# Performance work log

Hardware: AMD Instinct MI355X
Metric: run time of the kernel (lower is better)

Reference implementation:

```python
import math
import jax, jax.numpy as jnp
import numpy as np

HEADS = 16


def setup_inputs() -> dict:
    key = jax.random.key(0)
    k1, k2, k3 = jax.random.split(key, 3)
    bs, n_ctx, width = 2, 2048, 1024
    x = jax.random.normal(k1, (bs, n_ctx, width), dtype=jnp.float32)
    # init_scale=0.25 style small init for stability
    W_qkv = jax.random.normal(k2, (width, 3 * width), dtype=jnp.float32) * (0.25 / math.sqrt(width))
    b_qkv = jnp.zeros((3 * width,), dtype=jnp.float32)
    W_proj = jax.random.normal(k3, (width, width), dtype=jnp.float32) * (0.25 / math.sqrt(width))
    b_proj = jnp.zeros((width,), dtype=jnp.float32)
    return {"x": x, "W_qkv": W_qkv, "b_qkv": b_qkv, "W_proj": W_proj, "b_proj": b_proj}


def reference(x, W_qkv, b_qkv, W_proj, b_proj):
    bs, n_ctx, width = x.shape
    qkv = x @ W_qkv + b_qkv                     # [b, s, 3*width]
    attn_ch = width // HEADS                    # head dim
    qkv = qkv.reshape(bs, n_ctx, HEADS, 3 * attn_ch)
    q, k, v = jnp.split(qkv, 3, axis=-1)        # each [b, s, h, c]
    scale = 1.0 / math.sqrt(math.sqrt(attn_ch)) # applied to both q and k
    weight = jnp.einsum('bthc,bshc->bhts', q * scale, k * scale)
    weight = jax.nn.softmax(weight.astype(jnp.float32), axis=-1).astype(qkv.dtype)
    out = jnp.einsum('bhts,bshc->bthc', weight, v).reshape(bs, n_ctx, width)
    return out @ W_proj + b_proj
```

## Files before the change

### kernel.cpp

```cpp
#include <hip/hip_runtime.h>


using u16 = unsigned short;
typedef __attribute__((ext_vector_type(8))) short s16x8;
typedef __attribute__((ext_vector_type(4))) float f32x4;
typedef __attribute__((ext_vector_type(16))) float f32x16;

__device__ __forceinline__ u16 f2bf(float f) {
    unsigned x = __builtin_bit_cast(unsigned, f);
    x += 0x7fffu + ((x >> 16) & 1u);
    return (u16)(x >> 16);
}
__device__ __forceinline__ float bf2f(u16 u) {
    return __builtin_bit_cast(float, ((unsigned)u) << 16);
}

#define MFMA(a, b, c)   __builtin_amdgcn_mfma_f32_16x16x32_bf16((a), (b), (c), 0, 0, 0)
#define MFMA32(a, b, c) __builtin_amdgcn_mfma_f32_32x32x16_bf16((a), (b), (c), 0, 0, 0)


__global__ __launch_bounds__(256) void convert_split(const float* __restrict__ in,
                                                     u16* __restrict__ H, u16* __restrict__ L, int n) {
    int i = (blockIdx.x * 256 + threadIdx.x) * 4;
    if (i >= n) return;
    float4 v = *(const float4*)(in + i);
    u16 h0 = f2bf(v.x), h1 = f2bf(v.y), h2 = f2bf(v.z), h3 = f2bf(v.w);
    ushort4 hh = { h0, h1, h2, h3 };
    ushort4 ll = { f2bf(v.x - bf2f(h0)), f2bf(v.y - bf2f(h1)), f2bf(v.z - bf2f(h2)), f2bf(v.w - bf2f(h3)) };
    *(ushort4*)(H + i) = hh;
    *(ushort4*)(L + i) = ll;
}

__global__ __launch_bounds__(256) void transpose_split(const float* __restrict__ W,
                                                       u16* __restrict__ TH, u16* __restrict__ TL,
                                                       int K, int N) {
    __shared__ float st[32][33];
    int n0 = blockIdx.x * 32, k0 = blockIdx.y * 32;
    int c = threadIdx.x & 31, r8 = threadIdx.x >> 5;
#pragma unroll
    for (int i = 0; i < 4; ++i) {
        int r = r8 + i * 8;
        st[r][c] = W[(size_t)(k0 + r) * N + n0 + c];
    }
    __syncthreads();
#pragma unroll
    for (int i = 0; i < 4; ++i) {
        int r = r8 + i * 8;
        float v = st[c][r];
        u16 h = f2bf(v);
        TH[(size_t)(n0 + r) * K + k0 + c] = h;
        TL[(size_t)(n0 + r) * K + k0 + c] = f2bf(v - bf2f(h));
    }
}


template <int EPI>
__global__ __launch_bounds__(256, 2) void gemm_bf16x3(
    const u16* __restrict__ AH, const u16* __restrict__ AL,
    const u16* __restrict__ BTH, const u16* __restrict__ BTL,
    const float* __restrict__ bias,
    u16* __restrict__ Qs, u16* __restrict__ Kb, u16* __restrict__ Vp,
    float* __restrict__ Out) {
    const int K = 1024;
    __shared__ u16 sAh[128][40], sAl[128][40], sBh[128][40], sBl[128][40];

    int m0 = blockIdx.y * 128, n0 = blockIdx.x * 128;
    int tid = threadIdx.x, lane = tid & 63, wv = tid >> 6;
    int g = lane >> 4, c16 = lane & 15;
    int wm = wv >> 1, wn = wv & 1;

    f32x4 acc[4][4] = {};

    for (int kt = 0; kt < 32; ++kt) {
        int k0 = kt * 32;
        s16x8 ra[2], rla[2], rb[2], rlb[2];
#pragma unroll
        for (int i = 0; i < 2; ++i) {
            int cc = i * 256 + tid;
            int rr = cc >> 2, ko = (cc & 3) * 8;
            ra[i]  = *(const s16x8*)(AH  + (size_t)(m0 + rr) * K + k0 + ko);
            rla[i] = *(const s16x8*)(AL  + (size_t)(m0 + rr) * K + k0 + ko);
            rb[i]  = *(const s16x8*)(BTH + (size_t)(n0 + rr) * K + k0 + ko);
            rlb[i] = *(const s16x8*)(BTL + (size_t)(n0 + rr) * K + k0 + ko);
        }
        __syncthreads();
#pragma unroll
        for (int i = 0; i < 2; ++i) {
            int cc = i * 256 + tid;
            int rr = cc >> 2, ko = (cc & 3) * 8;
            *(s16x8*)&sAh[rr][ko] = ra[i];
            *(s16x8*)&sAl[rr][ko] = rla[i];
            *(s16x8*)&sBh[rr][ko] = rb[i];
            *(s16x8*)&sBl[rr][ko] = rlb[i];
        }
        __syncthreads();

        s16x8 ah[4], al[4], bh[4], bl[4];
#pragma unroll
        for (int mi = 0; mi < 4; ++mi) {
            ah[mi] = *(const s16x8*)&sAh[wm * 64 + mi * 16 + c16][g * 8];
            al[mi] = *(const s16x8*)&sAl[wm * 64 + mi * 16 + c16][g * 8];
        }
#pragma unroll
        for (int ni = 0; ni < 4; ++ni) {
            bh[ni] = *(const s16x8*)&sBh[wn * 64 + ni * 16 + c16][g * 8];
            bl[ni] = *(const s16x8*)&sBl[wn * 64 + ni * 16 + c16][g * 8];
        }
#pragma unroll
        for (int mi = 0; mi < 4; ++mi)
#pragma unroll
            for (int ni = 0; ni < 4; ++ni) {
                f32x4 c = acc[mi][ni];
                c = MFMA(ah[mi], bh[ni], c);
                c = MFMA(al[mi], bh[ni], c);
                c = MFMA(ah[mi], bl[ni], c);
                acc[mi][ni] = c;
            }
    }

#pragma unroll
    for (int ni = 0; ni < 4; ++ni) {
        int col = n0 + wn * 64 + ni * 16 + c16;
        float bs = bias[col];
        if (EPI == 0) {
            int h = col / 192;
            int rm = col - h * 192;
#pragma unroll
            for (int mi = 0; mi < 4; ++mi)
#pragma unroll
                for (int r = 0; r < 4; ++r) {
                    int row = m0 + wm * 64 + mi * 16 + 4 * g + r;
                    int b = row >> 11, s = row & 2047;
                    int bh16 = b * 16 + h;
                    float val = acc[mi][ni][r] + bs;
                    if (rm < 64)
                        Qs[(((size_t)bh16 * 2048 + s) << 6) + rm] = f2bf(val * 0.125f);
                    else if (rm < 128)
                        Kb[(((size_t)bh16 * 2048 + s) << 6) + rm - 64] = f2bf(val);
                    else {
                        int d = rm - 128;
                        int kg = s >> 4, k16 = s & 15;
                        int mm = (k16 & 3) | (((k16 >> 3) & 1) << 2) | (((k16 >> 2) & 1) << 3);
                        Vp[(((size_t)bh16 * 128 + kg) * 64 + d) * 16 + mm] = f2bf(val);
                    }
                }
        } else {
#pragma unroll
            for (int mi = 0; mi < 4; ++mi)
#pragma unroll
                for (int r = 0; r < 4; ++r) {
                    int row = m0 + wm * 64 + mi * 16 + 4 * g + r;
                    Out[(size_t)row * 1024 + col] = acc[mi][ni][r] + bs;
                }
        }
    }
}

__global__ __launch_bounds__(256, 2) void attn_fwd(
    const u16* __restrict__ Qs, const u16* __restrict__ Kb, const u16* __restrict__ Vp,
    u16* __restrict__ OH, u16* __restrict__ OL) {
    int id = blockIdx.x;
    int xcd = id & 7, li = id >> 3;
    int bh = xcd * 4 + (li >> 4);
    int qb = li & 15;
    int tid = threadIdx.x, w = tid >> 6, lane = tid & 63;
    int l31 = lane & 31, h = lane >> 5;
    int q0 = (qb * 4 + w) * 32;

    size_t base = (size_t)bh * 2048 * 64;
    size_t vbase = (size_t)bh * 128 * 64 * 16;

    const u16* qp = Qs + base + (size_t)(q0 + l31) * 64 + 8 * h;
    s16x8 qf0 = *(const s16x8*)(qp);
    s16x8 qf1 = *(const s16x8*)(qp + 16);
    s16x8 qf2 = *(const s16x8*)(qp + 32);
    s16x8 qf3 = *(const s16x8*)(qp + 48);

    const u16* kp = Kb + base + (size_t)l31 * 64 + 8 * h;
    const u16* vb = Vp + vbase + (size_t)l31 * 16 + 8 * h;

    f32x16 o0 = {}, o1 = {};
    float m = -1e30f, ls = 0.f;

    s16x8 ka0, ka1, ka2, ka3, kb0, kb1, kb2, kb3;
    ka0 = *(const s16x8*)(kp);
    ka1 = *(const s16x8*)(kp + 16);
    ka2 = *(const s16x8*)(kp + 32);
    ka3 = *(const s16x8*)(kp + 48);

    auto step = [&](s16x8& c0, s16x8& c1, s16x8& c2, s16x8& c3,
                    s16x8& n0, s16x8& n1, s16x8& n2, s16x8& n3,
                    int kv, int kvn) {
        const u16* vp = vb + (size_t)(kv >> 4) * 1024;
        s16x8 v00 = *(const s16x8*)(vp);
        s16x8 v10 = *(const s16x8*)(vp + 512);
        s16x8 v01 = *(const s16x8*)(vp + 1024);
        s16x8 v11 = *(const s16x8*)(vp + 1536);

        f32x16 s = {};
        s = MFMA32(c0, qf0, s);
        s = MFMA32(c1, qf1, s);
        s = MFMA32(c2, qf2, s);
        s = MFMA32(c3, qf3, s);

        const u16* kpn = kp + (size_t)kvn * 64;
        n0 = *(const s16x8*)(kpn);
        n1 = *(const s16x8*)(kpn + 16);
        n2 = *(const s16x8*)(kpn + 32);
        n3 = *(const s16x8*)(kpn + 48);

        float pmax = s[0];
#pragma unroll
        for (int r = 1; r < 16; ++r) pmax = fmaxf(pmax, s[r]);
        pmax = fmaxf(pmax, __shfl_xor(pmax, 32));

        if (!__all(pmax <= m + 8.f)) {
            float mn = fmaxf(m, pmax);
            float f = __expf(m - mn);
            m = mn;
            ls *= f;
#pragma unroll
            for (int r = 0; r < 16; ++r) {
                float fb = __shfl(f, (r & 3) + 8 * (r >> 2) + 4 * h);
                o0[r] *= fb;
                o1[r] *= fb;
            }
        }

        float sm = 0.f;
        u16 pb[16];
#pragma unroll
        for (int r = 0; r < 16; ++r) {
            float e = __expf(s[r] - m);
            sm += e;
            pb[r] = f2bf(e);
        }
        sm += __shfl_xor(sm, 32);
        ls += sm;

        s16x8 pa0, pa1;
#pragma unroll
        for (int e = 0; e < 8; ++e) {
            pa0[e] = (short)pb[e];
            pa1[e] = (short)pb[8 + e];
        }

        o0 = MFMA32(pa0, v00, o0);
        o0 = MFMA32(pa1, v01, o0);
        o1 = MFMA32(pa0, v10, o1);
        o1 = MFMA32(pa1, v11, o1);
    };

    for (int j = 0; j < 64; j += 2) {
        step(ka0, ka1, ka2, ka3, kb0, kb1, kb2, kb3, j * 32, (j + 1) * 32);
        step(kb0, kb1, kb2, kb3, ka0, ka1, ka2, ka3, (j + 1) * 32, ((j + 2) & 63) * 32);
    }

    int b = bh >> 4, hh = bh & 15;
    float inv = 1.0f / ls;
#pragma unroll
    for (int r = 0; r < 16; ++r) {
        int cr = (r & 3) + 8 * (r >> 2) + 4 * h;
        float fb = __shfl(inv, cr);
        int row = q0 + cr;
        size_t idx = ((size_t)(b * 2048 + row)) * 1024 + hh * 64 + l31;
        float v0 = o0[r] * fb, v1 = o1[r] * fb;
        u16 h0 = f2bf(v0);
        OH[idx] = h0;
        OL[idx] = f2bf(v0 - bf2f(h0));
        u16 h1 = f2bf(v1);
        OH[idx + 32] = h1;
        OL[idx + 32] = f2bf(v1 - bf2f(h1));
    }
}


extern "C" void kernel_launch(void* const* d_in, const int* in_sizes, int n_in,
                              void* d_out, int out_size, void* d_ws, size_t ws_size,
                              hipStream_t stream) {
    const float* x     = (const float*)d_in[0];
    const float* Wqkv  = (const float*)d_in[1];
    const float* bqkv  = (const float*)d_in[2];
    const float* Wproj = (const float*)d_in[3];
    const float* bproj = (const float*)d_in[4];
    float* out = (float*)d_out;

    char* w = (char*)d_ws;
    const size_t SZ_X  = (size_t)4096 * 1024 * 2;
    const size_t SZ_WQ = (size_t)3072 * 1024 * 2;
    const size_t SZ_WP = (size_t)1024 * 1024 * 2;
    u16* XH  = (u16*)w; w += SZ_X;
    u16* XL  = (u16*)w; w += SZ_X;
    u16* WQH = (u16*)w; w += SZ_WQ;
    u16* WQL = (u16*)w; w += SZ_WQ;
    u16* WPH = (u16*)w; w += SZ_WP;
    u16* WPL = (u16*)w; w += SZ_WP;
    u16* Q_s = (u16*)w; w += SZ_X;
    u16* K_b = (u16*)w; w += SZ_X;
    u16* V_p = (u16*)w; w += SZ_X;
    u16* OHp = (u16*)w; w += SZ_X;
    u16* OLp = (u16*)w; w += SZ_X;

    convert_split<<<4096, 256, 0, stream>>>(x, XH, XL, 4096 * 1024);
    transpose_split<<<dim3(96, 32), 256, 0, stream>>>(Wqkv, WQH, WQL, 1024, 3072);
    transpose_split<<<dim3(32, 32), 256, 0, stream>>>(Wproj, WPH, WPL, 1024, 1024);
    gemm_bf16x3<0><<<dim3(24, 32), 256, 0, stream>>>(XH, XL, WQH, WQL, bqkv, Q_s, K_b, V_p, nullptr);
    attn_fwd<<<512, 256, 0, stream>>>(Q_s, K_b, V_p, OHp, OLp);
    gemm_bf16x3<1><<<dim3(8, 32), 256, 0, stream>>>(OHp, OLp, WPH, WPL, bproj, nullptr, nullptr, nullptr, out);
}
```

Measured before the change: 214.2 us.

## Process 64 keys per attention step, fold log2e into Q, use exp2

```diff
diff --git a/kernel.cpp b/kernel.cpp
--- a/kernel.cpp
+++ b/kernel.cpp
@@ -13,6 +13,13 @@
 }
 __device__ __forceinline__ float bf2f(u16 u) {
     return __builtin_bit_cast(float, ((unsigned)u) << 16);
+}
+__device__ __forceinline__ unsigned pk2bf(float lo, float hi) {
+    unsigned a = __builtin_bit_cast(unsigned, lo);
+    unsigned b = __builtin_bit_cast(unsigned, hi);
+    a += 0x7fffu + ((a >> 16) & 1u);
+    b += 0x7fffu + ((b >> 16) & 1u);
+    return (a >> 16) | (b & 0xffff0000u);
 }
 
 #define MFMA(a, b, c)   __builtin_amdgcn_mfma_f32_16x16x32_bf16((a), (b), (c), 0, 0, 0)
@@ -134,7 +141,7 @@
                     int bh16 = b * 16 + h;
                     float val = acc[mi][ni][r] + bs;
                     if (rm < 64)
-                        Qs[(((size_t)bh16 * 2048 + s) << 6) + rm] = f2bf(val * 0.125f);
+                        Qs[(((size_t)bh16 * 2048 + s) << 6) + rm] = f2bf(val * 0.18033688011112042f);
                     else if (rm < 128)
                         Kb[(((size_t)bh16 * 2048 + s) << 6) + rm - 64] = f2bf(val);
                     else {
@@ -168,13 +175,12 @@
     int q0 = (qb * 4 + w) * 32;
 
     size_t base = (size_t)bh * 2048 * 64;
-    size_t vbase = (size_t)bh * 128 * 64 * 16;
+    size_t vbase = (size_t)bh * 131072;
 
     const u16* qp = Qs + base + (size_t)(q0 + l31) * 64 + 8 * h;
-    s16x8 qf0 = *(const s16x8*)(qp);
-    s16x8 qf1 = *(const s16x8*)(qp + 16);
-    s16x8 qf2 = *(const s16x8*)(qp + 32);
-    s16x8 qf3 = *(const s16x8*)(qp + 48);
+    s16x8 qf[4];
+#pragma unroll
+    for (int c = 0; c < 4; ++c) qf[c] = *(const s16x8*)(qp + 16 * c);
 
     const u16* kp = Kb + base + (size_t)l31 * 64 + 8 * h;
     const u16* vb = Vp + vbase + (size_t)l31 * 16 + 8 * h;
@@ -182,41 +188,53 @@
     f32x16 o0 = {}, o1 = {};
     float m = -1e30f, ls = 0.f;
 
-    s16x8 ka0, ka1, ka2, ka3, kb0, kb1, kb2, kb3;
-    ka0 = *(const s16x8*)(kp);
-    ka1 = *(const s16x8*)(kp + 16);
-    ka2 = *(const s16x8*)(kp + 32);
-    ka3 = *(const s16x8*)(kp + 48);
-
-    auto step = [&](s16x8& c0, s16x8& c1, s16x8& c2, s16x8& c3,
-                    s16x8& n0, s16x8& n1, s16x8& n2, s16x8& n3,
-                    int kv, int kvn) {
-        const u16* vp = vb + (size_t)(kv >> 4) * 1024;
-        s16x8 v00 = *(const s16x8*)(vp);
-        s16x8 v10 = *(const s16x8*)(vp + 512);
-        s16x8 v01 = *(const s16x8*)(vp + 1024);
-        s16x8 v11 = *(const s16x8*)(vp + 1536);
-
-        f32x16 s = {};
-        s = MFMA32(c0, qf0, s);
-        s = MFMA32(c1, qf1, s);
-        s = MFMA32(c2, qf2, s);
-        s = MFMA32(c3, qf3, s);
-
-        const u16* kpn = kp + (size_t)kvn * 64;
-        n0 = *(const s16x8*)(kpn);
-        n1 = *(const s16x8*)(kpn + 16);
-        n2 = *(const s16x8*)(kpn + 32);
-        n3 = *(const s16x8*)(kpn + 48);
-
-        float pmax = s[0];
-#pragma unroll
-        for (int r = 1; r < 16; ++r) pmax = fmaxf(pmax, s[r]);
+    s16x8 kA[8], kB[8];
+#pragma unroll
+    for (int i = 0; i < 8; ++i)
+        kA[i] = *(const s16x8*)(kp + (i >> 2) * 2048 + (i & 3) * 16);
+
+    auto step = [&](s16x8 (&cur)[8], s16x8 (&nxt)[8], int j) {
+        const u16* vp = vb + (size_t)j * 4096;
+        s16x8 v[8];
+#pragma unroll
+        for (int b = 0; b < 2; ++b)
+#pragma unroll
+            for (int hf = 0; hf < 2; ++hf)
+#pragma unroll
+                for (int n = 0; n < 2; ++n)
+                    v[b * 4 + hf * 2 + n] = *(const s16x8*)(vp + b * 2048 + hf * 1024 + n * 512);
+
+        f32x16 s0 = {}, s1 = {};
+        s0 = MFMA32(cur[0], qf[0], s0);
+        s0 = MFMA32(cur[1], qf[1], s0);
+        s0 = MFMA32(cur[2], qf[2], s0);
+        s0 = MFMA32(cur[3], qf[3], s0);
+        s1 = MFMA32(cur[4], qf[0], s1);
+        s1 = MFMA32(cur[5], qf[1], s1);
+        s1 = MFMA32(cur[6], qf[2], s1);
+        s1 = MFMA32(cur[7], qf[3], s1);
+
+        int jn = (j + 1) & 31;
+        const u16* kpn = kp + (size_t)jn * 4096;
+#pragma unroll
+        for (int i = 0; i < 8; ++i)
+            nxt[i] = *(const s16x8*)(kpn + (i >> 2) * 2048 + (i & 3) * 16);
+
+        float t0 = fmaxf(s0[0], s1[0]), t1 = fmaxf(s0[1], s1[1]);
+        float t2 = fmaxf(s0[2], s1[2]), t3 = fmaxf(s0[3], s1[3]);
+#pragma unroll
+        for (int r = 4; r < 16; r += 4) {
+            t0 = fmaxf(t0, fmaxf(s0[r], s1[r]));
+            t1 = fmaxf(t1, fmaxf(s0[r + 1], s1[r + 1]));
+            t2 = fmaxf(t2, fmaxf(s0[r + 2], s1[r + 2]));
+            t3 = fmaxf(t3, fmaxf(s0[r + 3], s1[r + 3]));
+        }
+        float pmax = fmaxf(fmaxf(t0, t1), fmaxf(t2, t3));
         pmax = fmaxf(pmax, __shfl_xor(pmax, 32));
 
         if (!__all(pmax <= m + 8.f)) {
             float mn = fmaxf(m, pmax);
-            float f = __expf(m - mn);
+            float f = __builtin_amdgcn_exp2f(m - mn);
             m = mn;
             ls *= f;
 #pragma unroll
@@ -227,33 +245,44 @@
             }
         }
 
-        float sm = 0.f;
-        u16 pb[16];
-#pragma unroll
-        for (int r = 0; r < 16; ++r) {
-            float e = __expf(s[r] - m);
-            sm += e;
-            pb[r] = f2bf(e);
-        }
+        float a0 = 0.f, a1 = 0.f, a2 = 0.f, a3 = 0.f;
+#pragma unroll
+        for (int r = 0; r < 16; r += 4) {
+            s0[r]     = __builtin_amdgcn_exp2f(s0[r] - m);     a0 += s0[r];
+            s0[r + 1] = __builtin_amdgcn_exp2f(s0[r + 1] - m); a1 += s0[r + 1];
+            s0[r + 2] = __builtin_amdgcn_exp2f(s0[r + 2] - m); a2 += s0[r + 2];
+            s0[r + 3] = __builtin_amdgcn_exp2f(s0[r + 3] - m); a3 += s0[r + 3];
+            s1[r]     = __builtin_amdgcn_exp2f(s1[r] - m);     a0 += s1[r];
+            s1[r + 1] = __builtin_amdgcn_exp2f(s1[r + 1] - m); a1 += s1[r + 1];
+            s1[r + 2] = __builtin_amdgcn_exp2f(s1[r + 2] - m); a2 += s1[r + 2];
+            s1[r + 3] = __builtin_amdgcn_exp2f(s1[r + 3] - m); a3 += s1[r + 3];
+        }
+        float sm = (a0 + a1) + (a2 + a3);
         sm += __shfl_xor(sm, 32);
         ls += sm;
 
-        s16x8 pa0, pa1;
-#pragma unroll
-        for (int e = 0; e < 8; ++e) {
-            pa0[e] = (short)pb[e];
-            pa1[e] = (short)pb[8 + e];
-        }
-
-        o0 = MFMA32(pa0, v00, o0);
-        o0 = MFMA32(pa1, v01, o0);
-        o1 = MFMA32(pa0, v10, o1);
-        o1 = MFMA32(pa1, v11, o1);
+        union { s16x8 v8; unsigned u[4]; } p00, p01, p10, p11;
+#pragma unroll
+        for (int k = 0; k < 4; ++k) {
+            p00.u[k] = pk2bf(s0[2 * k], s0[2 * k + 1]);
+            p01.u[k] = pk2bf(s0[8 + 2 * k], s0[9 + 2 * k]);
+            p10.u[k] = pk2bf(s1[2 * k], s1[2 * k + 1]);
+            p11.u[k] = pk2bf(s1[8 + 2 * k], s1[9 + 2 * k]);
+        }
+
+        o0 = MFMA32(p00.v8, v[0], o0);
+        o1 = MFMA32(p00.v8, v[1], o1);
+        o0 = MFMA32(p01.v8, v[2], o0);
+        o1 = MFMA32(p01.v8, v[3], o1);
+        o0 = MFMA32(p10.v8, v[4], o0);
+        o1 = MFMA32(p10.v8, v[5], o1);
+        o0 = MFMA32(p11.v8, v[6], o0);
+        o1 = MFMA32(p11.v8, v[7], o1);
     };
 
-    for (int j = 0; j < 64; j += 2) {
-        step(ka0, ka1, ka2, ka3, kb0, kb1, kb2, kb3, j * 32, (j + 1) * 32);
-        step(kb0, kb1, kb2, kb3, ka0, ka1, ka2, ka3, (j + 1) * 32, ((j + 2) & 63) * 32);
+    for (int j = 0; j < 32; j += 2) {
+        step(kA, kB, j);
+        step(kB, kA, j + 1);
     }
 
     int b = bh >> 4, hh = bh & 15;
```

Result: no change. 216.6 us (+1.1%).
